# Kernel optimization log

Measured on AMD Instinct MI355X. Metric: run time of the kernel, lower is better.

The kernel has to match this reference:

```python
import jax, jax.numpy as jnp
import numpy as np

HEADS = 8
N_STATE = 512
MAX_SEQ = 2048
DEPTH = N_STATE // HEADS
EPS = 1e-5


def layer_norm(x, g, b):
    mu = jnp.mean(x, axis=-1, keepdims=True)
    var = jnp.mean(jnp.square(x - mu), axis=-1, keepdims=True)
    return (x - mu) * jax.lax.rsqrt(var + EPS) * g + b


def setup_inputs() -> dict:
    key = jax.random.key(0)
    ks = jax.random.split(key, 12)
    B, S = 2, 2048
    x = jax.random.normal(ks[0], (B, S, N_STATE), dtype=jnp.float32)
    # causal additive mask (upper triangle = -1e9)
    mask = jnp.where(jnp.tril(jnp.ones((S, S), dtype=bool)), 0.0, -1e9).astype(jnp.float32)
    sc = 0.02
    Wqkv = jax.random.normal(ks[1], (N_STATE, 3 * N_STATE), dtype=jnp.float32) * sc
    bqkv = jnp.zeros((3 * N_STATE,), dtype=jnp.float32)
    Wproj = jax.random.normal(ks[2], (N_STATE, N_STATE), dtype=jnp.float32) * sc
    bproj = jnp.zeros((N_STATE,), dtype=jnp.float32)
    # xavier-normal-ish relative position embeddings, shape (H, max_seq, depth)
    E = jax.random.normal(ks[3], (HEADS, MAX_SEQ, DEPTH), dtype=jnp.float32) * (2.0 / (MAX_SEQ + DEPTH)) ** 0.5
    g1 = jnp.ones((N_STATE,), dtype=jnp.float32)
    b1 = jnp.zeros((N_STATE,), dtype=jnp.float32)
    g2 = jnp.ones((N_STATE,), dtype=jnp.float32)
    b2 = jnp.zeros((N_STATE,), dtype=jnp.float32)
    W1 = jax.random.normal(ks[4], (N_STATE, 4 * N_STATE), dtype=jnp.float32) * sc
    bm1 = jnp.zeros((4 * N_STATE,), dtype=jnp.float32)
    W2 = jax.random.normal(ks[5], (4 * N_STATE, N_STATE), dtype=jnp.float32) * sc
    bm2 = jnp.zeros((N_STATE,), dtype=jnp.float32)
    return {"x": x, "mask": mask, "Wqkv": Wqkv, "bqkv": bqkv, "Wproj": Wproj,
            "bproj": bproj, "E": E, "g1": g1, "b1": b1, "g2": g2, "b2": b2,
            "W1": W1, "bm1": bm1, "W2": W2, "bm2": bm2}


def relative_attn(q, E):
    # q: [B,H,S,D]; E: [H,max_seq,D] -> rel: [B,H,S,S] via skew trick
    B, H, S, D = q.shape
    Es = E[:, MAX_SEQ - S:]                      # [H,S,D]
    rel = jnp.einsum('bhsd,htd->bhst', q, Es)    # [B,H,S,S]
    rel = jnp.pad(rel, ((0, 0), (0, 0), (0, 0), (1, 0)))  # pad left of last dim
    rel = rel.reshape(B, H, S + 1, S)[:, :, 1:]  # skew: drop first row
    return rel


def reference(x, mask, Wqkv, bqkv, Wproj, bproj, E, g1, b1, g2, b2, W1, bm1, W2, bm2):
    B, S, _ = x.shape
    # --- attention sublayer ---
    a = layer_norm(x, g1, b1)
    qkv = a @ Wqkv + bqkv                        # [B,S,3*n_state]
    q, k, v = jnp.split(qkv, 3, axis=-1)
    def heads(t):
        return t.reshape(B, S, HEADS, DEPTH).transpose(0, 2, 1, 3)  # [B,H,S,D]
    q, k, v = heads(q), heads(k), heads(v)
    w = jnp.einsum('bhsd,bhtd->bhst', q, k) + relative_attn(q, E)
    w = w * (1.0 / jnp.sqrt(jnp.float32(DEPTH)))
    w = w + mask                                  # broadcast [S,S]
    w = jax.nn.softmax(w, axis=-1)
    att = jnp.einsum('bhst,bhtd->bhsd', w, v)
    att = att.transpose(0, 2, 1, 3).reshape(B, S, N_STATE)
    att = att @ Wproj + bproj
    x = x + att
    # --- MLP sublayer ---
    m = layer_norm(x, g2, b2)
    m = jax.nn.gelu(m @ W1 + bm1) @ W2 + bm2
    return x + m
```

## Files before the change

### kernel.cpp

```cpp
#include <hip/hip_runtime.h>
#include <math.h>

typedef unsigned short u16;
typedef unsigned int u32;
using short8 = __attribute__((ext_vector_type(8))) short;
using f32x4  = __attribute__((ext_vector_type(4))) float;

#define SEQ 2048
#define NH 8
#define DM 512
#define DH 64
#define NROWS 4096
#define BATCH 2
#define KVB 128

__device__ __forceinline__ float bf2f(u16 u) {
  union { u32 i; float f; } c; c.i = ((u32)u) << 16; return c.f;
}
__device__ __forceinline__ u16 f2bf(float f) {
  union { float f; u32 i; } c; c.f = f;
  u32 r = c.i + 0x7fffu + ((c.i >> 16) & 1u);
  return (u16)(r >> 16);
}

__device__ __forceinline__ void gll16(const u16* g, u16* l) {
  __builtin_amdgcn_global_load_lds(
      (const __attribute__((address_space(1))) u32*)g,
      (__attribute__((address_space(3))) u32*)l, 16, 0, 0);
}

template<int N> __device__ __forceinline__ void waitcnt_vm() {
  if constexpr (N == 0)      asm volatile("s_waitcnt vmcnt(0)" ::: "memory");
  else if constexpr (N == 4) asm volatile("s_waitcnt vmcnt(4)" ::: "memory");
  else if constexpr (N == 6) asm volatile("s_waitcnt vmcnt(6)" ::: "memory");
  else if constexpr (N == 8) asm volatile("s_waitcnt vmcnt(8)" ::: "memory");
}

__global__ __launch_bounds__(64) void ln_bf16_kernel(
    const float* __restrict__ x, const float* __restrict__ gw,
    const float* __restrict__ bw, u16* __restrict__ out)
{
  int row = blockIdx.x;
  int lane = threadIdx.x;
  const float* xr = x + (size_t)row * DM;
  float4 v0 = ((const float4*)xr)[lane];
  float4 v1 = ((const float4*)xr)[lane + 64];
  float s  = v0.x + v0.y + v0.z + v0.w + v1.x + v1.y + v1.z + v1.w;
  float s2 = v0.x*v0.x + v0.y*v0.y + v0.z*v0.z + v0.w*v0.w
           + v1.x*v1.x + v1.y*v1.y + v1.z*v1.z + v1.w*v1.w;
  #pragma unroll
  for (int m = 1; m < 64; m <<= 1) {
    s  += __shfl_xor(s,  m);
    s2 += __shfl_xor(s2, m);
  }
  float mu   = s * (1.0f / DM);
  float var  = s2 * (1.0f / DM) - mu * mu;
  float rstd = rsqrtf(var + 1e-5f);
  float4 ga = ((const float4*)gw)[lane],      ba = ((const float4*)bw)[lane];
  float4 gb = ((const float4*)gw)[lane + 64], bb = ((const float4*)bw)[lane + 64];
  ushort4 o0, o1;
  o0.x = f2bf((v0.x - mu) * rstd * ga.x + ba.x);
  o0.y = f2bf((v0.y - mu) * rstd * ga.y + ba.y);
  o0.z = f2bf((v0.z - mu) * rstd * ga.z + ba.z);
  o0.w = f2bf((v0.w - mu) * rstd * ga.w + ba.w);
  o1.x = f2bf((v1.x - mu) * rstd * gb.x + bb.x);
  o1.y = f2bf((v1.y - mu) * rstd * gb.y + bb.y);
  o1.z = f2bf((v1.z - mu) * rstd * gb.z + bb.z);
  o1.w = f2bf((v1.w - mu) * rstd * gb.w + bb.w);
  *(ushort4*)&out[(size_t)row * DM + lane * 4]       = o0;
  *(ushort4*)&out[(size_t)row * DM + 256 + lane * 4] = o1;
}

__global__ __launch_bounds__(256) void transpose_cast_kernel(
    const float* __restrict__ W, u16* __restrict__ Wt, int K, int N)
{
  __shared__ float tile[32][33];
  int bn = blockIdx.x * 32, bk = blockIdx.y * 32;
  int tx = threadIdx.x & 31, ty = threadIdx.x >> 5;
  #pragma unroll
  for (int i = 0; i < 32; i += 8)
    tile[ty + i][tx] = W[(size_t)(bk + ty + i) * N + bn + tx];
  __syncthreads();
  #pragma unroll
  for (int i = 0; i < 32; i += 8)
    Wt[(size_t)(bn + ty + i) * K + bk + tx] = f2bf(tile[tx][ty + i]);
}

__global__ __launch_bounds__(256) void cast_bf16_kernel(
    const float* __restrict__ in, u16* __restrict__ out, int n)
{
  int i = (blockIdx.x * 256 + threadIdx.x) * 4;
  if (i >= n) return;
  float4 v = *(const float4*)&in[i];
  ushort4 o;
  o.x = f2bf(v.x); o.y = f2bf(v.y); o.z = f2bf(v.z); o.w = f2bf(v.w);
  *(ushort4*)&out[i] = o;
}

template<int TM, int TN, int MODE>
__global__ __launch_bounds__(256) void gemm_bf16(
    const u16* __restrict__ A, const u16* __restrict__ Bt,
    const float* __restrict__ bias, const float* __restrict__ res,
    float* __restrict__ outF, u16* __restrict__ outB0,
    u16* __restrict__ outB1, u16* __restrict__ outB2,
    int M, int N, int K)
{
  constexpr int MI = TM / 32;
  constexpr int NI = TN / 32;
  constexpr int LOADS = TM / 32 + TN / 32;
  __shared__ u16 sA[2][TM * 64];
  __shared__ u16 sB[2][TN * 64];
  int tid = threadIdx.x;
  int lane = tid & 63, wv = tid >> 6;
  int wm = wv >> 1, wn = wv & 1;
  int g = lane >> 4, l15 = lane & 15;

  int nwg = gridDim.x, lin = blockIdx.x;
  int qq = nwg >> 3;
  int wg = (lin & 7) * qq + (lin >> 3);
  int ntn = N / TN;
  int m0 = (wg / ntn) * TM, n0 = (wg % ntn) * TN;

  auto stage = [&](int buf, int k0) {
    #pragma unroll
    for (int s = 0; s < TM / 32; ++s) {
      int c = s * 256 + tid;
      int row = c >> 3, p = c & 7;
      gll16(&A[(size_t)(m0 + row) * K + k0 + ((p ^ (row & 7)) * 8)],
            &sA[buf][(size_t)(s * 256 + wv * 64) * 8]);
    }
    #pragma unroll
    for (int s = 0; s < TN / 32; ++s) {
      int c = s * 256 + tid;
      int row = c >> 3, p = c & 7;
      gll16(&Bt[(size_t)(n0 + row) * K + k0 + ((p ^ (row & 7)) * 8)],
            &sB[buf][(size_t)(s * 256 + wv * 64) * 8]);
    }
  };

  f32x4 acc[MI][NI] = {};
  stage(0, 0);

  int nk = K / 64;
  for (int kt = 0; kt < nk; ++kt) {
    int cur = kt & 1;
    __syncthreads();
    if (kt + 1 < nk) {
      stage(cur ^ 1, (kt + 1) * 64);
      waitcnt_vm<LOADS>();
    } else {
      waitcnt_vm<0>();
    }
    __syncthreads();
    #pragma unroll
    for (int kk = 0; kk < 2; ++kk) {
      short8 af[MI], bfr[NI];
      #pragma unroll
      for (int i = 0; i < MI; ++i) {
        int row = wm * (TM / 2) + i * 16 + l15;
        af[i] = *(const short8*)&sA[cur][row * 64 + (((4 * kk + g) ^ (row & 7)) * 8)];
      }
      #pragma unroll
      for (int i = 0; i < NI; ++i) {
        int row = wn * (TN / 2) + i * 16 + l15;
        bfr[i] = *(const short8*)&sB[cur][row * 64 + (((4 * kk + g) ^ (row & 7)) * 8)];
      }
      #pragma unroll
      for (int mi = 0; mi < MI; ++mi)
        #pragma unroll
        for (int ni = 0; ni < NI; ++ni)
          acc[mi][ni] = __builtin_amdgcn_mfma_f32_16x16x32_bf16(af[mi], bfr[ni], acc[mi][ni], 0, 0, 0);
    }
  }

  #pragma unroll
  for (int mi = 0; mi < MI; ++mi) {
    #pragma unroll
    for (int ni = 0; ni < NI; ++ni) {
      #pragma unroll
      for (int r = 0; r < 4; ++r) {
        int grow = m0 + wm * (TM / 2) + mi * 16 + g * 4 + r;
        int gcol = n0 + wn * (TN / 2) + ni * 16 + l15;
        float val = acc[mi][ni][r] + bias[gcol];
        if (MODE == 0) {
          int part = gcol >> 9, c = gcol & 511;
          int hh = c >> 6, dd = c & 63;
          int bb = grow >> 11, ss = grow & 2047;
          size_t dst = (((size_t)(bb * NH + hh)) * SEQ + ss) * DH + dd;
          if (part == 0)      outB0[dst] = f2bf(val * 0.18033688011112042f);
          else if (part == 1) outB1[dst] = f2bf(val);
          else                outB2[dst] = f2bf(val);
        } else if (MODE == 1 || MODE == 3) {
          size_t idx = (size_t)grow * DM + gcol;
          outF[idx] = val + res[idx];
        } else {
          float t = val;
          float inner = 0.7978845608028654f * (t + 0.044715f * t * t * t);
          float gl = 0.5f * t * (1.0f + tanhf(inner));
          outB0[(size_t)grow * N + gcol] = f2bf(gl);
        }
      }
    }
  }
}

__global__ __launch_bounds__(256, 2) void attn_kernel(
    const u16* __restrict__ Q, const u16* __restrict__ Kb,
    const u16* __restrict__ Vb, const u16* __restrict__ Eb,
    u16* __restrict__ Ob)
{
  __shared__ u16 sK[KVB * 64];
  __shared__ u16 sV[64 * (KVB + 8)];
  __shared__ u16 sP[4][16 * 64];
  __shared__ float sM[2][32];
  __shared__ float sS[2][32];

  int tid = threadIdx.x, lane = tid & 63, wv = tid >> 6;
  int wr = wv & 1, wc = wv >> 1;
  int g = lane >> 4, l15 = lane & 15;
  int lin = blockIdx.x;
  int blk = (lin & 7) * 64 + (lin >> 3);
  int bh = blk >> 5, pp = blk & 31;
  int hh = bh & (NH - 1), bb = bh >> 3;

  const u16* Qh = Q  + (size_t)bh * SEQ * DH;
  const u16* Kh = Kb + (size_t)bh * SEQ * DH;
  const u16* Vh = Vb + (size_t)bh * SEQ * DH;
  const u16* Eh = Eb + (size_t)hh * SEQ * DH;

  int tileA = pp, tileB = 63 - pp;
  int itersA = pp / 4 + 1;
  const int TOT = 17;

  int rstage = tid >> 3, cstage = (tid & 7) * 8;

  #pragma unroll
  for (int s = 0; s < 4; ++s) {
    int c = s * 256 + tid, t = c >> 3, pc = c & 7;
    gll16(&Kh[(size_t)t * DH + ((pc ^ (t & 7)) * 8)],
          &sK[(size_t)(s * 256 + wv * 64) * 8]);
  }
  #pragma unroll
  for (int q = 0; q < 4; ++q) {
    int t = q * 32 + rstage;
    short8 vv = *(const short8*)&Vh[(size_t)t * DH + cstage];
    #pragma unroll
    for (int j = 0; j < 8; ++j) {
      int d = cstage + j;
      sV[d * (KVB + 8) + (((t >> 3) ^ (d >> 3)) * 8) + (t & 7)] = (u16)vv[j];
    }
  }
  asm volatile("s_waitcnt vmcnt(0)" ::: "memory");
  __syncthreads();

  short8 qf[2];
  {
    int sw = tileA * 32 + wr * 16;
    qf[0] = *(const short8*)&Qh[(size_t)(sw + l15) * DH + g * 8];
    qf[1] = *(const short8*)&Qh[(size_t)(sw + l15) * DH + g * 8 + 32];
  }
  f32x4 o[4] = {};
  float mrow[4] = {-1e30f, -1e30f, -1e30f, -1e30f};
  float lsum[4] = {};

  float* sO = (float*)&sP[0][0];

  auto flushOut = [&](int tile) {
    int swt = tile * 32 + wr * 16;
    if (wc == 1) {
      #pragma unroll
      for (int r = 0; r < 4; ++r) {
        float rl = 1.0f / lsum[r];
        #pragma unroll
        for (int nb = 0; nb < 4; ++nb)
          sO[wr * 1024 + (g * 4 + r) * 64 + nb * 16 + l15] = o[nb][r] * rl;
      }
    }
    __syncthreads();
    if (wc == 0) {
      #pragma unroll
      for (int r = 0; r < 4; ++r) {
        float rl = 1.0f / lsum[r];
        int ss = swt + g * 4 + r;
        #pragma unroll
        for (int nb = 0; nb < 4; ++nb) {
          float val = o[nb][r] * rl + sO[wr * 1024 + (g * 4 + r) * 64 + nb * 16 + l15];
          Ob[((size_t)(bb * SEQ + ss)) * DM + hh * DH + nb * 16 + l15] = f2bf(val);
        }
      }
    }
  };

  for (int it = 0; it < TOT; ++it) {
    if (it == itersA) {
      flushOut(tileA);
      #pragma unroll
      for (int nb = 0; nb < 4; ++nb) o[nb] = f32x4{};
      #pragma unroll
      for (int r = 0; r < 4; ++r) { mrow[r] = -1e30f; lsum[r] = 0.f; }
      int sw = tileB * 32 + wr * 16;
      qf[0] = *(const short8*)&Qh[(size_t)(sw + l15) * DH + g * 8];
      qf[1] = *(const short8*)&Qh[(size_t)(sw + l15) * DH + g * 8 + 32];
    }
    int tile = (it < itersA) ? tileA : tileB;
    int kt   = (it < itersA) ? it : it - itersA;
    int sw = tile * 32 + wr * 16, t0 = kt * KVB;

    bool pre = (it + 1 < TOT);
    int tb = 0;
    short8 vp[4];
    if (pre) {
      int kn = (it + 1 < itersA) ? it + 1 : it + 1 - itersA;
      tb = kn * KVB;
      #pragma unroll
      for (int q = 0; q < 4; ++q)
        vp[q] = *(const short8*)&Vh[(size_t)(tb + q * 32 + rstage) * DH + cstage];
    }

    f32x4 accS[4];
    #pragma unroll
    for (int ni = 0; ni < 4; ++ni) {
      int row = wc * 64 + ni * 16 + l15;
      short8 k0 = *(const short8*)&sK[row * 64 + ((g ^ (row & 7)) * 8)];
      short8 k1 = *(const short8*)&sK[row * 64 + (((4 + g) ^ (row & 7)) * 8)];
      f32x4 z = {};
      z = __builtin_amdgcn_mfma_f32_16x16x32_bf16(qf[0], k0, z, 0, 0, 0);
      z = __builtin_amdgcn_mfma_f32_16x16x32_bf16(qf[1], k1, z, 0, 0, 0);
      accS[ni] = z;
    }

    int jbase = 2032 - sw + t0 + wc * 64;
    f32x4 accR[5];
    #pragma unroll
    for (int nb = 0; nb < 5; ++nb) {
      int j = jbase + nb * 16 + l15; if (j > 2047) j = 2047;
      short8 e0 = *(const short8*)&Eh[(size_t)j * DH + g * 8];
      short8 e1 = *(const short8*)&Eh[(size_t)j * DH + 32 + g * 8];
      f32x4 z = {};
      z = __builtin_amdgcn_mfma_f32_16x16x32_bf16(qf[0], e0, z, 0, 0, 0);
      z = __builtin_amdgcn_mfma_f32_16x16x32_bf16(qf[1], e1, z, 0, 0, 0);
      accR[nb] = z;
    }

    bool needMask = (t0 + wc * 64 + 63 > sw);
    #pragma unroll
    for (int r = 0; r < 4; ++r) {
      int srow = g * 4 + r;
      int dsh = 15 - srow + l15;
      int srcl = (lane & 48) + (dsh & 15);
      float sh[5];
      #pragma unroll
      for (int nb = 0; nb < 5; ++nb) sh[nb] = __shfl(accR[nb][r], srcl);
      bool cy = dsh >= 16;
      #pragma unroll
      for (int ni = 0; ni < 4; ++ni) {
        float rel = cy ? sh[ni + 1] : sh[ni];
        float val = accS[ni][r] + rel;
        if (needMask && (t0 + wc * 64 + ni * 16 + l15 > sw + srow)) val = -1e30f;
        accS[ni][r] = val;
      }
    }

    float lmax[4];
    #pragma unroll
    for (int r = 0; r < 4; ++r) {
      float tm = fmaxf(fmaxf(accS[0][r], accS[1][r]), fmaxf(accS[2][r], accS[3][r]));
      tm = fmaxf(tm, __shfl_xor(tm, 1));
      tm = fmaxf(tm, __shfl_xor(tm, 2));
      tm = fmaxf(tm, __shfl_xor(tm, 4));
      tm = fmaxf(tm, __shfl_xor(tm, 8));
      lmax[r] = tm;
    }
    if (l15 == 0) {
      #pragma unroll
      for (int r = 0; r < 4; ++r) sM[wc][wr * 16 + g * 4 + r] = lmax[r];
    }
    __syncthreads();
    if (pre) {
      #pragma unroll
      for (int s = 0; s < 4; ++s) {
        int c = s * 256 + tid, t = c >> 3, pc = c & 7;
        gll16(&Kh[(size_t)(tb + t) * DH + ((pc ^ (t & 7)) * 8)],
              &sK[(size_t)(s * 256 + wv * 64) * 8]);
      }
    }
    float4 om = *(float4*)&sM[wc ^ 1][wr * 16 + g * 4];

    float sesav[4], lscl[4];
    #pragma unroll
    for (int r = 0; r < 4; ++r) {
      float gm = fmaxf(lmax[r], ((float*)&om)[r]);
      float mnew = fmaxf(mrow[r], gm);
      lscl[r] = exp2f(mrow[r] - mnew);
      mrow[r] = mnew;
      float se = 0.f;
      #pragma unroll
      for (int ni = 0; ni < 4; ++ni) {
        float pe = exp2f(accS[ni][r] - mnew);
        accS[ni][r] = pe;
        se += pe;
      }
      se += __shfl_xor(se, 1); se += __shfl_xor(se, 2);
      se += __shfl_xor(se, 4); se += __shfl_xor(se, 8);
      sesav[r] = se;
      o[0][r] *= lscl[r]; o[1][r] *= lscl[r]; o[2][r] *= lscl[r]; o[3][r] *= lscl[r];
    }
    if (l15 == 0) {
      #pragma unroll
      for (int r = 0; r < 4; ++r) sS[wc][wr * 16 + g * 4 + r] = sesav[r];
    }

    #pragma unroll
    for (int ni = 0; ni < 4; ++ni)
      #pragma unroll
      for (int r = 0; r < 4; ++r) {
        int srow = g * 4 + r;
        int chunk = (ni * 2 + (l15 >> 3)) ^ (srow & 7);
        sP[wv][srow * 64 + chunk * 8 + (l15 & 7)] = f2bf(accS[ni][r]);
      }
    asm volatile("s_waitcnt lgkmcnt(0)" ::: "memory");
    __builtin_amdgcn_sched_barrier(0);
    #pragma unroll
    for (int kk = 0; kk < 2; ++kk) {
      short8 pf = *(const short8*)&sP[wv][l15 * 64 + (((kk * 4 + g) ^ (l15 & 7)) * 8)];
      #pragma unroll
      for (int nb = 0; nb < 4; ++nb) {
        int d = nb * 16 + l15;
        int ck = wc * 8 + kk * 4 + g;
        short8 vf = *(const short8*)&sV[d * (KVB + 8) + ((ck ^ (d >> 3)) * 8)];
        o[nb] = __builtin_amdgcn_mfma_f32_16x16x32_bf16(pf, vf, o[nb], 0, 0, 0);
      }
    }

    __syncthreads();
    float4 os = *(float4*)&sS[wc ^ 1][wr * 16 + g * 4];
    #pragma unroll
    for (int r = 0; r < 4; ++r)
      lsum[r] = lsum[r] * lscl[r] + sesav[r] + ((float*)&os)[r];

    if (pre) {
      #pragma unroll
      for (int q = 0; q < 4; ++q) {
        int t = q * 32 + rstage;
        #pragma unroll
        for (int j = 0; j < 8; ++j) {
          int d = cstage + j;
          sV[d * (KVB + 8) + (((t >> 3) ^ (d >> 3)) * 8) + (t & 7)] = (u16)vp[q][j];
        }
      }
    }
  }

  flushOut(tileB);
}

extern "C" void kernel_launch(void* const* d_in, const int* in_sizes, int n_in,
                              void* d_out, int out_size, void* d_ws, size_t ws_size,
                              hipStream_t stream) {
  const float* x     = (const float*)d_in[0];
  const float* Wqkv  = (const float*)d_in[2];
  const float* bqkv  = (const float*)d_in[3];
  const float* Wproj = (const float*)d_in[4];
  const float* bproj = (const float*)d_in[5];
  const float* E     = (const float*)d_in[6];
  const float* g1    = (const float*)d_in[7];
  const float* b1    = (const float*)d_in[8];
  const float* g2    = (const float*)d_in[9];
  const float* b2    = (const float*)d_in[10];
  const float* W1    = (const float*)d_in[11];
  const float* bm1   = (const float*)d_in[12];
  const float* W2    = (const float*)d_in[13];
  const float* bm2   = (const float*)d_in[14];
  float* out = (float*)d_out;

  char* ws = (char*)d_ws;
  size_t off = 0;
  auto alloc = [&](size_t bytes) {
    void* p = ws + off;
    off += (bytes + 255) & ~(size_t)255;
    return p;
  };
  u16* a_bf   = (u16*)alloc((size_t)NROWS * DM * 2);
  u16* q_bf   = (u16*)alloc((size_t)NROWS * DM * 2);
  u16* k_bf   = (u16*)alloc((size_t)NROWS * DM * 2);
  u16* v_bf   = (u16*)alloc((size_t)NROWS * DM * 2);
  u16* att_bf = (u16*)alloc((size_t)NROWS * DM * 2);
  float* y    = (float*)alloc((size_t)NROWS * DM * 4);
  u16* h_bf   = (u16*)alloc((size_t)NROWS * 2048 * 2);
  u16* WqkvT  = (u16*)alloc((size_t)1536 * 512 * 2);
  u16* WprojT = (u16*)alloc((size_t)512 * 512 * 2);
  u16* W1T    = (u16*)alloc((size_t)2048 * 512 * 2);
  u16* W2T    = (u16*)alloc((size_t)512 * 2048 * 2);
  u16* E_bf   = (u16*)alloc((size_t)NH * SEQ * DH * 2);

  transpose_cast_kernel<<<dim3(1536 / 32, 512 / 32), 256, 0, stream>>>(Wqkv, WqkvT, 512, 1536);
  transpose_cast_kernel<<<dim3(512 / 32, 512 / 32), 256, 0, stream>>>(Wproj, WprojT, 512, 512);
  transpose_cast_kernel<<<dim3(2048 / 32, 512 / 32), 256, 0, stream>>>(W1, W1T, 512, 2048);
  transpose_cast_kernel<<<dim3(512 / 32, 2048 / 32), 256, 0, stream>>>(W2, W2T, 2048, 512);
  cast_bf16_kernel<<<(NH * SEQ * DH) / (256 * 4), 256, 0, stream>>>(E, E_bf, NH * SEQ * DH);

  ln_bf16_kernel<<<NROWS, 64, 0, stream>>>(x, g1, b1, a_bf);
  gemm_bf16<64, 128, 0><<<(NROWS / 64) * (1536 / 128), 256, 0, stream>>>(
      a_bf, WqkvT, bqkv, nullptr, nullptr, q_bf, k_bf, v_bf, NROWS, 1536, 512);
  attn_kernel<<<512, 256, 0, stream>>>(q_bf, k_bf, v_bf, E_bf, att_bf);
  gemm_bf16<64, 64, 1><<<(NROWS / 64) * (512 / 64), 256, 0, stream>>>(
      att_bf, WprojT, bproj, x, y, nullptr, nullptr, nullptr, NROWS, 512, 512);
  ln_bf16_kernel<<<NROWS, 64, 0, stream>>>(y, g2, b2, a_bf);
  gemm_bf16<64, 128, 2><<<(NROWS / 64) * (2048 / 128), 256, 0, stream>>>(
      a_bf, W1T, bm1, nullptr, nullptr, h_bf, nullptr, nullptr, NROWS, 2048, 512);
  gemm_bf16<64, 64, 3><<<(NROWS / 64) * (512 / 64), 256, 0, stream>>>(
      h_bf, W2T, bm2, y, out, nullptr, nullptr, nullptr, NROWS, 512, 2048);
}
```

Measured before the change: 168.7 us.

## Replace paired causal tiles with one query tile per block, heaviest first

The attention kernel used to give each block two query tiles (pp and 63-pp) so every block did the same 17 KV iterations for causal load balance. Now each block handles a single 32-row query tile, and the grid doubles to 1024 blocks. Blocks are ordered from the largest tile down so the longest-running blocks start first. This exposes more parallelism and removes the mid-loop flush and reset, but blocks now differ in work and each block repeats its own K/V prologue.

```diff
diff --git a/kernel.cpp b/kernel.cpp
--- a/kernel.cpp
+++ b/kernel.cpp
@@ -219,19 +219,16 @@
   int wr = wv & 1, wc = wv >> 1;
   int g = lane >> 4, l15 = lane & 15;
   int lin = blockIdx.x;
-  int blk = (lin & 7) * 64 + (lin >> 3);
-  int bh = blk >> 5, pp = blk & 31;
+  int bh   = (lin & 7) * 2 + ((lin >> 3) & 1);
+  int tile = 63 - (lin >> 4);
   int hh = bh & (NH - 1), bb = bh >> 3;
+  int NIT = tile / 4 + 1;
 
   const u16* Qh = Q  + (size_t)bh * SEQ * DH;
   const u16* Kh = Kb + (size_t)bh * SEQ * DH;
   const u16* Vh = Vb + (size_t)bh * SEQ * DH;
   const u16* Eh = Eb + (size_t)hh * SEQ * DH;
 
-  int tileA = pp, tileB = 63 - pp;
-  int itersA = pp / 4 + 1;
-  const int TOT = 17;
-
   int rstage = tid >> 3, cstage = (tid & 7) * 8;
 
   #pragma unroll
@@ -253,65 +250,24 @@
   asm volatile("s_waitcnt vmcnt(0)" ::: "memory");
   __syncthreads();
 
+  int sw = tile * 32 + wr * 16;
   short8 qf[2];
-  {
-    int sw = tileA * 32 + wr * 16;
-    qf[0] = *(const short8*)&Qh[(size_t)(sw + l15) * DH + g * 8];
-    qf[1] = *(const short8*)&Qh[(size_t)(sw + l15) * DH + g * 8 + 32];
-  }
+  qf[0] = *(const short8*)&Qh[(size_t)(sw + l15) * DH + g * 8];
+  qf[1] = *(const short8*)&Qh[(size_t)(sw + l15) * DH + g * 8 + 32];
+
   f32x4 o[4] = {};
   float mrow[4] = {-1e30f, -1e30f, -1e30f, -1e30f};
   float lsum[4] = {};
 
   float* sO = (float*)&sP[0][0];
 
-  auto flushOut = [&](int tile) {
-    int swt = tile * 32 + wr * 16;
-    if (wc == 1) {
-      #pragma unroll
-      for (int r = 0; r < 4; ++r) {
-        float rl = 1.0f / lsum[r];
-        #pragma unroll
-        for (int nb = 0; nb < 4; ++nb)
-          sO[wr * 1024 + (g * 4 + r) * 64 + nb * 16 + l15] = o[nb][r] * rl;
-      }
-    }
-    __syncthreads();
-    if (wc == 0) {
-      #pragma unroll
-      for (int r = 0; r < 4; ++r) {
-        float rl = 1.0f / lsum[r];
-        int ss = swt + g * 4 + r;
-        #pragma unroll
-        for (int nb = 0; nb < 4; ++nb) {
-          float val = o[nb][r] * rl + sO[wr * 1024 + (g * 4 + r) * 64 + nb * 16 + l15];
-          Ob[((size_t)(bb * SEQ + ss)) * DM + hh * DH + nb * 16 + l15] = f2bf(val);
-        }
-      }
-    }
-  };
-
-  for (int it = 0; it < TOT; ++it) {
-    if (it == itersA) {
-      flushOut(tileA);
-      #pragma unroll
-      for (int nb = 0; nb < 4; ++nb) o[nb] = f32x4{};
-      #pragma unroll
-      for (int r = 0; r < 4; ++r) { mrow[r] = -1e30f; lsum[r] = 0.f; }
-      int sw = tileB * 32 + wr * 16;
-      qf[0] = *(const short8*)&Qh[(size_t)(sw + l15) * DH + g * 8];
-      qf[1] = *(const short8*)&Qh[(size_t)(sw + l15) * DH + g * 8 + 32];
-    }
-    int tile = (it < itersA) ? tileA : tileB;
-    int kt   = (it < itersA) ? it : it - itersA;
-    int sw = tile * 32 + wr * 16, t0 = kt * KVB;
-
-    bool pre = (it + 1 < TOT);
-    int tb = 0;
+  for (int it = 0; it < NIT; ++it) {
+    int t0 = it * KVB;
+    bool pre = (it + 1 < NIT);
+    int tb = (it + 1) * KVB;
+
     short8 vp[4];
     if (pre) {
-      int kn = (it + 1 < itersA) ? it + 1 : it + 1 - itersA;
-      tb = kn * KVB;
       #pragma unroll
       for (int q = 0; q < 4; ++q)
         vp[q] = *(const short8*)&Vh[(size_t)(tb + q * 32 + rstage) * DH + cstage];
@@ -451,7 +407,30 @@
     }
   }
 
-  flushOut(tileB);
+  {
+    if (wc == 1) {
+      #pragma unroll
+      for (int r = 0; r < 4; ++r) {
+        float rl = 1.0f / lsum[r];
+        #pragma unroll
+        for (int nb = 0; nb < 4; ++nb)
+          sO[wr * 1024 + (g * 4 + r) * 64 + nb * 16 + l15] = o[nb][r] * rl;
+      }
+    }
+    __syncthreads();
+    if (wc == 0) {
+      #pragma unroll
+      for (int r = 0; r < 4; ++r) {
+        float rl = 1.0f / lsum[r];
+        int ss = sw + g * 4 + r;
+        #pragma unroll
+        for (int nb = 0; nb < 4; ++nb) {
+          float val = o[nb][r] * rl + sO[wr * 1024 + (g * 4 + r) * 64 + nb * 16 + l15];
+          Ob[((size_t)(bb * SEQ + ss)) * DM + hh * DH + nb * 16 + l15] = f2bf(val);
+        }
+      }
+    }
+  }
 }
 
 extern "C" void kernel_launch(void* const* d_in, const int* in_sizes, int n_in,
@@ -502,7 +481,7 @@
   ln_bf16_kernel<<<NROWS, 64, 0, stream>>>(x, g1, b1, a_bf);
   gemm_bf16<64, 128, 0><<<(NROWS / 64) * (1536 / 128), 256, 0, stream>>>(
       a_bf, WqkvT, bqkv, nullptr, nullptr, q_bf, k_bf, v_bf, NROWS, 1536, 512);
-  attn_kernel<<<512, 256, 0, stream>>>(q_bf, k_bf, v_bf, E_bf, att_bf);
+  attn_kernel<<<1024, 256, 0, stream>>>(q_bf, k_bf, v_bf, E_bf, att_bf);
   gemm_bf16<64, 64, 1><<<(NROWS / 64) * (512 / 64), 256, 0, stream>>>(
       att_bf, WprojT, bproj, x, y, nullptr, nullptr, nullptr, NROWS, 512, 512);
   ln_bf16_kernel<<<NROWS, 64, 0, stream>>>(y, g2, b2, a_bf);
```

Result: no change. 168.1 us (-0.3%).
